# Optimization experiments

Measured on AMD Instinct MI355X. Metric: run time of the kernel, lower is better.

## Reference

```python
import jax, jax.numpy as jnp
import numpy as np

N_NODES = 100000
N_EDGES = 1000000
N_GRAPHS = 256
NUM_NODE_TYPES = 200
EMB_DIM = 64
HID_DIM = 32


def _gcn_conv(x, src, dst, W, b, n):
    """PyG GCNConv: x' = D^-1/2 (A+I) D^-1/2 (x W) + b. src/dst already include self-loops."""
    xw = x @ W  # [n, out]
    ones = jnp.ones(dst.shape, dtype=xw.dtype)
    deg = jax.ops.segment_sum(ones, dst, num_segments=n)  # in-degree incl. self-loop
    dinv = jnp.where(deg > 0, jax.lax.rsqrt(jnp.maximum(deg, 1e-12)), 0.0)
    norm = dinv[src] * dinv[dst]  # [E+n]
    msg = xw[src] * norm[:, None]  # gather + scale
    return jax.ops.segment_sum(msg, dst, num_segments=n) + b


def setup_inputs() -> dict:
    key = jax.random.key(0)
    ks = jax.random.split(key, 12)
    x = jax.random.randint(ks[0], (N_NODES, 1), 0, NUM_NODE_TYPES, dtype=jnp.int64)
    edge_index = jax.random.randint(ks[1], (2, N_EDGES), 0, N_NODES, dtype=jnp.int64)
    batch = jnp.sort(jax.random.randint(ks[2], (N_NODES,), 0, N_GRAPHS, dtype=jnp.int64))
    s = 0.05
    emb = jax.random.normal(ks[3], (NUM_NODE_TYPES, EMB_DIM), dtype=jnp.float32)
    W1 = jax.random.normal(ks[4], (EMB_DIM, HID_DIM), dtype=jnp.float32) * s
    b1 = jnp.zeros((HID_DIM,), dtype=jnp.float32)
    W2 = jax.random.normal(ks[5], (HID_DIM, HID_DIM), dtype=jnp.float32) * s
    b2 = jnp.zeros((HID_DIM,), dtype=jnp.float32)
    Wc1 = jax.random.normal(ks[6], (HID_DIM, 16), dtype=jnp.float32) * s
    bc1 = jnp.zeros((16,), dtype=jnp.float32)
    Wc2 = jax.random.normal(ks[7], (16, 1), dtype=jnp.float32) * s
    bc2 = jnp.zeros((1,), dtype=jnp.float32)
    return dict(x=x, edge_index=edge_index, batch=batch, emb=emb, W1=W1, b1=b1,
                W2=W2, b2=b2, Wc1=Wc1, bc1=bc1, Wc2=Wc2, bc2=bc2)


def reference(x, edge_index, batch, emb, W1, b1, W2, b2, Wc1, bc1, Wc2, bc2):
    n = x.shape[0]
    ids = x[:, 0]  # x.squeeze()
    loops = jnp.arange(n, dtype=edge_index.dtype)
    src = jnp.concatenate([edge_index[0], loops])
    dst = jnp.concatenate([edge_index[1], loops])

    h = emb[ids]  # [N, 64] embedding lookup
    h = jax.nn.relu(_gcn_conv(h, src, dst, W1, b1, n))
    h = jax.nn.relu(_gcn_conv(h, src, dst, W2, b2, n))

    # global_mean_pool over batch segments
    seg_sum = jax.ops.segment_sum(h, batch, num_segments=N_GRAPHS)
    counts = jax.ops.segment_sum(jnp.ones((n,), dtype=h.dtype), batch, num_segments=N_GRAPHS)
    pooled = seg_sum / jnp.maximum(counts, 1.0)[:, None]  # [B, 32]

    hc = jax.nn.relu(pooled @ Wc1 + bc1)
    return jax.nn.sigmoid(hc @ Wc2 + bc2)  # [B, 1]
```

## Files before the change

kernel.cpp:

```cpp
#include <hip/hip_runtime.h>
#include <math.h>

#define N_NODES   100000
#define N_EDGES   1000000
#define N_GRAPHS  256
#define NUM_TYPES 200
#define EMB       64
#define HID       32

#define BSHIFT    8
#define BSTRIDE   256
#define NBUCK     ((N_NODES + BSTRIDE - 1) / BSTRIDE)
#define EPB       4096
#define NBINBLK   ((N_EDGES + EPB - 1) / EPB)
#define MAXBE     4096
#define SRCBITS   17
#define SRCMASK   0x1FFFF


__global__ __launch_bounds__(256) void k_binA(const int* __restrict__ dst,
                                              int* __restrict__ counts) {
    __shared__ int cnt[NBUCK];
    int tid = threadIdx.x, k = blockIdx.x;
    for (int b = tid; b < NBUCK; b += 256) cnt[b] = 0;
    __syncthreads();
    int base = k * EPB;
    int n = min(EPB, N_EDGES - base);
    for (int t = tid; t < n; t += 256) atomicAdd(&cnt[dst[base + t] >> BSHIFT], 1);
    __syncthreads();
    for (int b = tid; b < NBUCK; b += 256) counts[k * NBUCK + b] = cnt[b];
}

__global__ __launch_bounds__(512) void k_misc(const int* __restrict__ counts,
                                              int* __restrict__ offs,
                                              int* __restrict__ bbase,
                                              const float* __restrict__ emb,
                                              const float* __restrict__ W1,
                                              float* __restrict__ table,
                                              float* __restrict__ pooled) {
    int tid = threadIdx.x;
    if (blockIdx.x == 0) {
        __shared__ int sA[512], sB[512];
        int total = 0;
        if (tid < NBUCK)
            for (int k = 0; k < NBINBLK; ++k) total += counts[k * NBUCK + tid];
        sA[tid] = (tid < NBUCK) ? total : 0;
        __syncthreads();
        int* in = sA; int* out = sB;
        for (int off = 1; off < 512; off <<= 1) {
            out[tid] = in[tid] + (tid >= off ? in[tid - off] : 0);
            __syncthreads();
            int* tmp = in; in = out; out = tmp;
        }
        int excl = in[tid] - ((tid < NBUCK) ? total : 0);
        if (tid < NBUCK) {
            bbase[tid] = excl;
            int run = excl;
            for (int k = 0; k < NBINBLK; ++k) {
                offs[k * NBUCK + tid] = run;
                run += counts[k * NBUCK + tid];
            }
        }
        if (tid == 0) bbase[NBUCK] = N_EDGES;
    } else if (blockIdx.x == 1) {
        for (int t = tid; t < NUM_TYPES * HID; t += 512) {
            int ty = t / HID, j = t % HID;
            float s = 0.f;
            for (int k = 0; k < EMB; ++k) s = fmaf(emb[ty * EMB + k], W1[k * HID + j], s);
            table[t] = s;
        }
    } else {
        for (int t = tid; t < N_GRAPHS * HID; t += 512) pooled[t] = 0.f;
    }
}

__global__ __launch_bounds__(256) void k_binB(const int* __restrict__ src,
                                              const int* __restrict__ dst,
                                              const int* __restrict__ offs,
                                              int* __restrict__ binned) {
    __shared__ int srcl[EPB];
    __shared__ int dstl[EPB];
    __shared__ unsigned short rank16[EPB];
    __shared__ unsigned short perm[EPB];
    __shared__ int cnt[NBUCK];
    __shared__ int loc[NBUCK];
    __shared__ int offsL[NBUCK];
    __shared__ int sA[512], sB[512];
    int tid = threadIdx.x, k = blockIdx.x;
    int base = k * EPB;
    int n = min(EPB, N_EDGES - base);
    for (int b = tid; b < NBUCK; b += 256) { cnt[b] = 0; offsL[b] = offs[k * NBUCK + b]; }
    __syncthreads();
    for (int t = tid; t < n; t += 256) {
        int s = src[base + t], d = dst[base + t];
        srcl[t] = s; dstl[t] = d;
        rank16[t] = (unsigned short)atomicAdd(&cnt[d >> BSHIFT], 1);
    }
    __syncthreads();
    for (int t = tid; t < 512; t += 256) sA[t] = (t < NBUCK) ? cnt[t] : 0;
    __syncthreads();
    int* in = sA; int* out = sB;
    for (int off = 1; off < 512; off <<= 1) {
        for (int t = tid; t < 512; t += 256)
            out[t] = in[t] + (t >= off ? in[t - off] : 0);
        __syncthreads();
        int* tmp = in; in = out; out = tmp;
    }
    for (int b = tid; b < NBUCK; b += 256) loc[b] = in[b] - cnt[b];
    __syncthreads();
    for (int t = tid; t < n; t += 256) {
        int b = dstl[t] >> BSHIFT;
        perm[loc[b] + rank16[t]] = (unsigned short)t;
    }
    __syncthreads();
    for (int t = tid; t < n; t += 256) {
        int e = perm[t];
        int d = dstl[e], b = d >> BSHIFT;
        int gpos = offsL[b] + (t - loc[b]);
        binned[gpos] = ((d & (BSTRIDE - 1)) << SRCBITS) | srcl[e];
    }
}

__global__ __launch_bounds__(256) void k_csr(const int* __restrict__ binned,
                                             const int* __restrict__ bbase,
                                             const int* __restrict__ ids,
                                             int* __restrict__ ssrc,
                                             int* __restrict__ row_ptr,
                                             float* __restrict__ dinv,
                                             int2* __restrict__ nodeinfo) {
    __shared__ int pk[MAXBE];
    __shared__ unsigned char dl[MAXBE];
    __shared__ unsigned short rank16[MAXBE];
    __shared__ unsigned short perm[MAXBE];
    __shared__ int degL[BSTRIDE];
    __shared__ int loc[BSTRIDE];
    __shared__ int sA[BSTRIDE], sB[BSTRIDE];
    int tid = threadIdx.x, b = blockIdx.x;
    int e0 = bbase[b], e1 = bbase[b + 1];
    int n = min(e1 - e0, MAXBE);
    degL[tid] = 0;
    __syncthreads();
    for (int t = tid; t < n; t += 256) {
        int v = binned[e0 + t];
        pk[t] = v;
        int d = v >> SRCBITS;
        dl[t] = (unsigned char)d;
        rank16[t] = (unsigned short)atomicAdd(&degL[d], 1);
    }
    __syncthreads();
    sA[tid] = degL[tid];
    __syncthreads();
    int* in = sA; int* out = sB;
    for (int off = 1; off < 256; off <<= 1) {
        out[tid] = in[tid] + (tid >= off ? in[tid - off] : 0);
        __syncthreads();
        int* tmp = in; in = out; out = tmp;
    }
    loc[tid] = in[tid] - degL[tid];
    __syncthreads();
    for (int t = tid; t < n; t += 256)
        perm[loc[dl[t]] + rank16[t]] = (unsigned short)t;
    __syncthreads();
    for (int t = tid; t < n; t += 256)
        ssrc[e0 + t] = pk[perm[t]] & SRCMASK;
    int i = b * BSTRIDE + tid;
    if (i < N_NODES) {
        row_ptr[i] = e0 + loc[tid];
        float dv = rsqrtf((float)degL[tid] + 1.0f);
        dinv[i] = dv;
        nodeinfo[i] = make_int2(ids[i], __float_as_int(dv));
    }
    if (b == NBUCK - 1 && tid == 0) row_ptr[N_NODES] = N_EDGES;
}


__global__ __launch_bounds__(256) void k_gather1(
        const int2* __restrict__ nodeinfo, const float* __restrict__ table,
        const int* __restrict__ row_ptr, const int* __restrict__ ssrc,
        const float* __restrict__ b1, const float* __restrict__ W2,
        float4* __restrict__ Y2) {
    __shared__ float w[HID * HID];
    for (int k = threadIdx.x; k < HID * HID; k += 256) w[k] = W2[k];
    __syncthreads();

    int t = blockIdx.x * 256 + threadIdx.x;
    int i = t >> 3, p = t & 7;
    const float4* tab4 = (const float4*)table;

    int s0 = row_ptr[i], n = row_ptr[i + 1] - s0;
    int2 self = nodeinfo[i];
    float di = __int_as_float(self.y);
    float4 acc = tab4[self.x * 8 + p];
    acc.x *= di; acc.y *= di; acc.z *= di; acc.w *= di;

    for (int e = 0; e < n; e += 8) {
        int ss[8];
        int2 ni[8];
#pragma unroll
        for (int u = 0; u < 8; ++u) {
            int idx = e + u; idx = (idx > n - 1) ? n - 1 : idx;
            ss[u] = ssrc[s0 + idx];
        }
#pragma unroll
        for (int u = 0; u < 8; ++u) ni[u] = nodeinfo[ss[u]];
#pragma unroll
        for (int u = 0; u < 8; ++u) {
            float ds = (e + u < n) ? __int_as_float(ni[u].y) : 0.f;
            float4 v = tab4[ni[u].x * 8 + p];
            acc.x = fmaf(v.x, ds, acc.x);
            acc.y = fmaf(v.y, ds, acc.y);
            acc.z = fmaf(v.z, ds, acc.z);
            acc.w = fmaf(v.w, ds, acc.w);
        }
    }
    float4 bb = ((const float4*)b1)[p];
    float4 h;
    h.x = fmaxf(fmaf(di, acc.x, bb.x), 0.f);
    h.y = fmaxf(fmaf(di, acc.y, bb.y), 0.f);
    h.z = fmaxf(fmaf(di, acc.z, bb.z), 0.f);
    h.w = fmaxf(fmaf(di, acc.w, bb.w), 0.f);

    float o0 = 0.f, o1 = 0.f, o2 = 0.f, o3 = 0.f;
    const float4* w4 = (const float4*)w;
#pragma unroll
    for (int q = 0; q < 8; ++q) {
        float4 hq;
        hq.x = __shfl(h.x, q, 8);
        hq.y = __shfl(h.y, q, 8);
        hq.z = __shfl(h.z, q, 8);
        hq.w = __shfl(h.w, q, 8);
        float4 w0 = w4[(4 * q + 0) * 8 + p];
        float4 w1 = w4[(4 * q + 1) * 8 + p];
        float4 w2 = w4[(4 * q + 2) * 8 + p];
        float4 w3 = w4[(4 * q + 3) * 8 + p];
        o0 = fmaf(hq.x, w0.x, o0); o1 = fmaf(hq.x, w0.y, o1); o2 = fmaf(hq.x, w0.z, o2); o3 = fmaf(hq.x, w0.w, o3);
        o0 = fmaf(hq.y, w1.x, o0); o1 = fmaf(hq.y, w1.y, o1); o2 = fmaf(hq.y, w1.z, o2); o3 = fmaf(hq.y, w1.w, o3);
        o0 = fmaf(hq.z, w2.x, o0); o1 = fmaf(hq.z, w2.y, o1); o2 = fmaf(hq.z, w2.z, o2); o3 = fmaf(hq.z, w2.w, o3);
        o0 = fmaf(hq.w, w3.x, o0); o1 = fmaf(hq.w, w3.y, o1); o2 = fmaf(hq.w, w3.z, o2); o3 = fmaf(hq.w, w3.w, o3);
    }
    float4 yv;
    yv.x = o0 * di; yv.y = o1 * di; yv.z = o2 * di; yv.w = o3 * di;
    Y2[i * 8 + p] = yv;
}

__global__ __launch_bounds__(256) void k_gather2(
        const float4* __restrict__ Y2, const int* __restrict__ row_ptr,
        const int* __restrict__ ssrc, const float* __restrict__ dinv,
        const float* __restrict__ b2, const int* __restrict__ batch,
        float* __restrict__ pooled) {
    __shared__ float lp[32][HID];
    for (int k = threadIdx.x; k < 32 * HID; k += 256) ((float*)lp)[k] = 0.f;
    __syncthreads();

    int t = blockIdx.x * 256 + threadIdx.x;
    int i = t >> 3, p = t & 7;
    int i0 = (blockIdx.x * 256) >> 3;
    int gFirst = batch[i0];

    float4 acc = Y2[i * 8 + p];
    int s0 = row_ptr[i], n = row_ptr[i + 1] - s0;
    for (int e = 0; e < n; e += 8) {
        int ss[8];
#pragma unroll
        for (int u = 0; u < 8; ++u) {
            int idx = e + u; idx = (idx > n - 1) ? n - 1 : idx;
            ss[u] = ssrc[s0 + idx];
        }
        float4 v[8];
#pragma unroll
        for (int u = 0; u < 8; ++u) v[u] = Y2[ss[u] * 8 + p];
#pragma unroll
        for (int u = 0; u < 8; ++u) {
            float wg = (e + u < n) ? 1.f : 0.f;
            acc.x = fmaf(v[u].x, wg, acc.x);
            acc.y = fmaf(v[u].y, wg, acc.y);
            acc.z = fmaf(v[u].z, wg, acc.z);
            acc.w = fmaf(v[u].w, wg, acc.w);
        }
    }
    float di = dinv[i];
    float4 bb = ((const float4*)b2)[p];
    float4 h;
    h.x = fmaxf(fmaf(di, acc.x, bb.x), 0.f);
    h.y = fmaxf(fmaf(di, acc.y, bb.y), 0.f);
    h.z = fmaxf(fmaf(di, acc.z, bb.z), 0.f);
    h.w = fmaxf(fmaf(di, acc.w, bb.w), 0.f);

    int gl = batch[i] - gFirst;
    atomicAdd(&lp[gl][p * 4 + 0], h.x);
    atomicAdd(&lp[gl][p * 4 + 1], h.y);
    atomicAdd(&lp[gl][p * 4 + 2], h.z);
    atomicAdd(&lp[gl][p * 4 + 3], h.w);
    __syncthreads();

    int gLast = batch[i0 + 31];
    int ng = gLast - gFirst + 1;
    for (int k = threadIdx.x; k < ng * HID; k += 256) {
        float v = lp[k / HID][k % HID];
        if (v != 0.f) atomicAdd(&pooled[(gFirst + k / HID) * HID + (k % HID)], v);
    }
}

__global__ void k_head(const float* __restrict__ pooled, const int* __restrict__ batch,
                       const float* __restrict__ Wc1, const float* __restrict__ bc1,
                       const float* __restrict__ Wc2, const float* __restrict__ bc2,
                       float* __restrict__ out) {
    int g = blockIdx.x * blockDim.x + threadIdx.x;
    if (g >= N_GRAPHS) return;
    int lo = 0, hi = N_NODES;
    while (lo < hi) { int mid = (lo + hi) >> 1; if (batch[mid] < g) lo = mid + 1; else hi = mid; }
    int start = lo;
    hi = N_NODES;
    while (lo < hi) { int mid = (lo + hi) >> 1; if (batch[mid] < g + 1) lo = mid + 1; else hi = mid; }
    int end = lo;
    float inv = 1.0f / fmaxf((float)(end - start), 1.0f);
    float m[HID];
    for (int j = 0; j < HID; ++j) m[j] = pooled[g * HID + j] * inv;
    float hc[16];
    for (int j = 0; j < 16; ++j) {
        float s = bc1[j];
        for (int k = 0; k < HID; ++k) s = fmaf(m[k], Wc1[k * 16 + j], s);
        hc[j] = fmaxf(s, 0.f);
    }
    float s = bc2[0];
    for (int k = 0; k < 16; ++k) s = fmaf(hc[k], Wc2[k], s);
    out[g] = 1.0f / (1.0f + expf(-s));
}


extern "C" void kernel_launch(void* const* d_in, const int* in_sizes, int n_in,
                              void* d_out, int out_size, void* d_ws, size_t ws_size,
                              hipStream_t stream) {
    const int*   ids  = (const int*)d_in[0];
    const int*   src  = (const int*)d_in[1];
    const int*   dst  = ((const int*)d_in[1]) + N_EDGES;
    const int*   batch = (const int*)d_in[2];
    const float* emb  = (const float*)d_in[3];
    const float* W1   = (const float*)d_in[4];
    const float* b1   = (const float*)d_in[5];
    const float* W2   = (const float*)d_in[6];
    const float* b2   = (const float*)d_in[7];
    const float* Wc1  = (const float*)d_in[8];
    const float* bc1  = (const float*)d_in[9];
    const float* Wc2  = (const float*)d_in[10];
    const float* bc2  = (const float*)d_in[11];
    float* out = (float*)d_out;

    float* Y2      = (float*)d_ws;
    int*   binned  = (int*)(Y2 + (size_t)N_NODES * HID);
    int*   ssrc    = binned + N_EDGES;
    int2*  nodeinfo = (int2*)(ssrc + N_EDGES);
    int*   counts  = (int*)(nodeinfo + N_NODES);
    int*   offs    = counts + NBINBLK * NBUCK;
    int*   bbase   = offs + NBINBLK * NBUCK;
    int*   row_ptr = bbase + NBUCK + 1;
    float* dinv    = (float*)(row_ptr + N_NODES + 2);
    float* table   = dinv + N_NODES;
    float* pooled  = table + NUM_TYPES * HID;

    const int B = 256;
    const int gNode8 = (N_NODES * 8) / B;

    k_binA<<<NBINBLK, B, 0, stream>>>(dst, counts);
    k_misc<<<3, 512, 0, stream>>>(counts, offs, bbase, emb, W1, table, pooled);
    k_binB<<<NBINBLK, B, 0, stream>>>(src, dst, offs, binned);
    k_csr<<<NBUCK, B, 0, stream>>>(binned, bbase, ids, ssrc, row_ptr, dinv, nodeinfo);

    k_gather1<<<gNode8, B, 0, stream>>>(nodeinfo, table, row_ptr, ssrc, b1, W2,
                                        (float4*)Y2);
    k_gather2<<<gNode8, B, 0, stream>>>((const float4*)Y2, row_ptr, ssrc, dinv, b2,
                                        batch, pooled);
    k_head<<<1, N_GRAPHS, 0, stream>>>(pooled, batch, Wc1, bc1, Wc2, bc2, out);
}
```

Measured before the change: 127.3 us.

## Precompute packed per-edge type/dinv info and store layer-2 features in fp16

Adds a pass that precomputes, per CSR edge, a packed word holding the source node's type id and its fp16 normalisation factor. This removes the dependent nodeinfo gather from the layer-1 inner loop. The intermediate Y2 features are also stored as fp16 (8 bytes per lane instead of 16), roughly halving gather traffic in layer 2. In exchange it adds an extra kernel launch and an edge pass, and introduces fp16 rounding of dinv and the hidden features.

New measurement: 126.0 us. No clear change (-1.0%).

```diff
diff --git a/kernel.cpp b/kernel.cpp
--- a/kernel.cpp
+++ b/kernel.cpp
@@ -1,4 +1,5 @@
 #include <hip/hip_runtime.h>
+#include <hip/hip_fp16.h>
 #include <math.h>
 
 #define N_NODES   100000
@@ -173,12 +174,28 @@
     if (b == NBUCK - 1 && tid == 0) row_ptr[N_NODES] = N_EDGES;
 }
 
+__global__ __launch_bounds__(256) void k_einfo(const int* __restrict__ ssrc,
+                                               const int2* __restrict__ nodeinfo,
+                                               unsigned int* __restrict__ einfo) {
+    int e0 = (blockIdx.x * 256 + threadIdx.x) * 4;
+    if (e0 >= N_EDGES) return;
+    int4 s4 = *(const int4*)(ssrc + e0);
+    int2 n0 = nodeinfo[s4.x], n1 = nodeinfo[s4.y];
+    int2 n2 = nodeinfo[s4.z], n3 = nodeinfo[s4.w];
+    uint4 r;
+    r.x = ((unsigned)n0.x << 16) | __half_as_ushort(__float2half(__int_as_float(n0.y)));
+    r.y = ((unsigned)n1.x << 16) | __half_as_ushort(__float2half(__int_as_float(n1.y)));
+    r.z = ((unsigned)n2.x << 16) | __half_as_ushort(__float2half(__int_as_float(n2.y)));
+    r.w = ((unsigned)n3.x << 16) | __half_as_ushort(__float2half(__int_as_float(n3.y)));
+    *(uint4*)(einfo + e0) = r;
+}
+
 
 __global__ __launch_bounds__(256) void k_gather1(
         const int2* __restrict__ nodeinfo, const float* __restrict__ table,
-        const int* __restrict__ row_ptr, const int* __restrict__ ssrc,
+        const int* __restrict__ row_ptr, const unsigned int* __restrict__ einfo,
         const float* __restrict__ b1, const float* __restrict__ W2,
-        float4* __restrict__ Y2) {
+        uint2* __restrict__ Y2h) {
     __shared__ float w[HID * HID];
     for (int k = threadIdx.x; k < HID * HID; k += 256) w[k] = W2[k];
     __syncthreads();
@@ -194,19 +211,17 @@
     acc.x *= di; acc.y *= di; acc.z *= di; acc.w *= di;
 
     for (int e = 0; e < n; e += 8) {
-        int ss[8];
-        int2 ni[8];
+        unsigned int ei[8];
 #pragma unroll
         for (int u = 0; u < 8; ++u) {
             int idx = e + u; idx = (idx > n - 1) ? n - 1 : idx;
-            ss[u] = ssrc[s0 + idx];
-        }
-#pragma unroll
-        for (int u = 0; u < 8; ++u) ni[u] = nodeinfo[ss[u]];
+            ei[u] = einfo[s0 + idx];
+        }
 #pragma unroll
         for (int u = 0; u < 8; ++u) {
-            float ds = (e + u < n) ? __int_as_float(ni[u].y) : 0.f;
-            float4 v = tab4[ni[u].x * 8 + p];
+            float ds = (e + u < n)
+                ? __half2float(__ushort_as_half((unsigned short)(ei[u] & 0xFFFF))) : 0.f;
+            float4 v = tab4[(ei[u] >> 16) * 8 + p];
             acc.x = fmaf(v.x, ds, acc.x);
             acc.y = fmaf(v.y, ds, acc.y);
             acc.z = fmaf(v.z, ds, acc.z);
@@ -238,13 +253,16 @@
         o0 = fmaf(hq.z, w2.x, o0); o1 = fmaf(hq.z, w2.y, o1); o2 = fmaf(hq.z, w2.z, o2); o3 = fmaf(hq.z, w2.w, o3);
         o0 = fmaf(hq.w, w3.x, o0); o1 = fmaf(hq.w, w3.y, o1); o2 = fmaf(hq.w, w3.z, o2); o3 = fmaf(hq.w, w3.w, o3);
     }
-    float4 yv;
-    yv.x = o0 * di; yv.y = o1 * di; yv.z = o2 * di; yv.w = o3 * di;
-    Y2[i * 8 + p] = yv;
+    __half2 h01 = __halves2half2(__float2half(o0 * di), __float2half(o1 * di));
+    __half2 h23 = __halves2half2(__float2half(o2 * di), __float2half(o3 * di));
+    uint2 wv;
+    wv.x = *(unsigned int*)&h01;
+    wv.y = *(unsigned int*)&h23;
+    Y2h[i * 8 + p] = wv;
 }
 
 __global__ __launch_bounds__(256) void k_gather2(
-        const float4* __restrict__ Y2, const int* __restrict__ row_ptr,
+        const uint2* __restrict__ Y2h, const int* __restrict__ row_ptr,
         const int* __restrict__ ssrc, const float* __restrict__ dinv,
         const float* __restrict__ b2, const int* __restrict__ batch,
         float* __restrict__ pooled) {
@@ -257,7 +275,11 @@
     int i0 = (blockIdx.x * 256) >> 3;
     int gFirst = batch[i0];
 
-    float4 acc = Y2[i * 8 + p];
+    uint2 selfv = Y2h[i * 8 + p];
+    float2 sa = __half22float2(*(__half2*)&selfv.x);
+    float2 sb = __half22float2(*(__half2*)&selfv.y);
+    float4 acc = make_float4(sa.x, sa.y, sb.x, sb.y);
+
     int s0 = row_ptr[i], n = row_ptr[i + 1] - s0;
     for (int e = 0; e < n; e += 8) {
         int ss[8];
@@ -266,16 +288,18 @@
             int idx = e + u; idx = (idx > n - 1) ? n - 1 : idx;
             ss[u] = ssrc[s0 + idx];
         }
-        float4 v[8];
-#pragma unroll
-        for (int u = 0; u < 8; ++u) v[u] = Y2[ss[u] * 8 + p];
+        uint2 v[8];
+#pragma unroll
+        for (int u = 0; u < 8; ++u) v[u] = Y2h[ss[u] * 8 + p];
 #pragma unroll
         for (int u = 0; u < 8; ++u) {
             float wg = (e + u < n) ? 1.f : 0.f;
-            acc.x = fmaf(v[u].x, wg, acc.x);
-            acc.y = fmaf(v[u].y, wg, acc.y);
-            acc.z = fmaf(v[u].z, wg, acc.z);
-            acc.w = fmaf(v[u].w, wg, acc.w);
+            float2 fa = __half22float2(*(__half2*)&v[u].x);
+            float2 fb = __half22float2(*(__half2*)&v[u].y);
+            acc.x = fmaf(fa.x, wg, acc.x);
+            acc.y = fmaf(fa.y, wg, acc.y);
+            acc.z = fmaf(fb.x, wg, acc.z);
+            acc.w = fmaf(fb.y, wg, acc.w);
         }
     }
     float di = dinv[i];
@@ -346,10 +370,11 @@
     const float* bc2  = (const float*)d_in[11];
     float* out = (float*)d_out;
 
-    float* Y2      = (float*)d_ws;
-    int*   binned  = (int*)(Y2 + (size_t)N_NODES * HID);
+    uint2* Y2h     = (uint2*)d_ws;
+    int*   binned  = (int*)(Y2h + (size_t)N_NODES * 8);
     int*   ssrc    = binned + N_EDGES;
-    int2*  nodeinfo = (int2*)(ssrc + N_EDGES);
+    unsigned int* einfo = (unsigned int*)(ssrc + N_EDGES);
+    int2*  nodeinfo = (int2*)(einfo + N_EDGES);
     int*   counts  = (int*)(nodeinfo + N_NODES);
     int*   offs    = counts + NBINBLK * NBUCK;
     int*   bbase   = offs + NBINBLK * NBUCK;
@@ -365,10 +390,10 @@
     k_misc<<<3, 512, 0, stream>>>(counts, offs, bbase, emb, W1, table, pooled);
     k_binB<<<NBINBLK, B, 0, stream>>>(src, dst, offs, binned);
     k_csr<<<NBUCK, B, 0, stream>>>(binned, bbase, ids, ssrc, row_ptr, dinv, nodeinfo);
-
-    k_gather1<<<gNode8, B, 0, stream>>>(nodeinfo, table, row_ptr, ssrc, b1, W2,
-                                        (float4*)Y2);
-    k_gather2<<<gNode8, B, 0, stream>>>((const float4*)Y2, row_ptr, ssrc, dinv, b2,
+    k_einfo<<<(N_EDGES / 4 + B - 1) / B, B, 0, stream>>>(ssrc, nodeinfo, einfo);
+
+    k_gather1<<<gNode8, B, 0, stream>>>(nodeinfo, table, row_ptr, einfo, b1, W2, Y2h);
+    k_gather2<<<gNode8, B, 0, stream>>>((const uint2*)Y2h, row_ptr, ssrc, dinv, b2,
                                         batch, pooled);
     k_head<<<1, N_GRAPHS, 0, stream>>>(pooled, batch, Wc1, bc1, Wc2, bc2, out);
 }
```
